# Kernel tuning notes

Measured on AMD Instinct MI355X. Metric: run time of the kernel, lower is better.

The kernel has to match this reference:

```python
import jax, jax.numpy as jnp
import numpy as np

B, S, D = 2, 2048, 1024
H = 16
HD = D // H
MLP = 4096
EPS = 1e-6


def _layernorm(x, g, b):
    mu = jnp.mean(x, axis=-1, keepdims=True)
    var = jnp.var(x, axis=-1, keepdims=True)
    return (x - mu) * jax.lax.rsqrt(var + EPS) * g + b


def setup_inputs() -> dict:
    key = jax.random.key(0)
    ks = jax.random.split(key, 16)
    sd = 1.0 / np.sqrt(D)
    sm = 1.0 / np.sqrt(MLP)
    return {
        "x": jax.random.normal(ks[0], (B, S, D), jnp.float32),
        "ln1_g": jnp.ones((D,), jnp.float32),
        "ln1_b": jnp.zeros((D,), jnp.float32),
        "wq": jax.random.normal(ks[1], (D, D), jnp.float32) * sd,
        "bq": jnp.zeros((D,), jnp.float32),
        "wk": jax.random.normal(ks[2], (D, D), jnp.float32) * sd,
        "bk": jnp.zeros((D,), jnp.float32),
        "wv": jax.random.normal(ks[3], (D, D), jnp.float32) * sd,
        "bv": jnp.zeros((D,), jnp.float32),
        "wo": jax.random.normal(ks[4], (D, D), jnp.float32) * sd,
        "bo": jnp.zeros((D,), jnp.float32),
        "ln2_g": jnp.ones((D,), jnp.float32),
        "ln2_b": jnp.zeros((D,), jnp.float32),
        "w1": jax.random.normal(ks[5], (D, MLP), jnp.float32) * sd,
        "b1": jnp.zeros((MLP,), jnp.float32),
        "w2": jax.random.normal(ks[6], (MLP, D), jnp.float32) * sm,
        "b2": jnp.zeros((D,), jnp.float32),
    }


def reference(x, ln1_g, ln1_b, wq, bq, wk, bk, wv, bv, wo, bo,
              ln2_g, ln2_b, w1, b1, w2, b2):
    # --- attention sub-block (pre-LN) ---
    h = _layernorm(x, ln1_g, ln1_b)
    q = (h @ wq + bq).reshape(B, S, H, HD).transpose(0, 2, 1, 3)  # [B,H,S,HD]
    k = (h @ wk + bk).reshape(B, S, H, HD).transpose(0, 2, 1, 3)
    v = (h @ wv + bv).reshape(B, S, H, HD).transpose(0, 2, 1, 3)
    scale = HD ** -0.5
    attn = jax.nn.softmax(jnp.einsum('bhqd,bhkd->bhqk', q, k) * scale, axis=-1)
    out = jnp.einsum('bhqk,bhkd->bhqd', attn, v)
    out = out.transpose(0, 2, 1, 3).reshape(B, S, D)
    x = x + (out @ wo + bo)
    # --- MLP sub-block (pre-LN) ---
    h = _layernorm(x, ln2_g, ln2_b)
    h = jax.nn.gelu(h @ w1 + b1, approximate=False)
    x = x + (h @ w2 + b2)
    return x
```

## Files before the change

### kernel.cpp

```cpp
#include <hip/hip_runtime.h>
#include <hip/hip_bf16.h>

typedef unsigned short u16;
typedef unsigned int u32;
typedef __attribute__((ext_vector_type(8))) unsigned short us8;
typedef __attribute__((ext_vector_type(4))) unsigned short us4;
typedef __attribute__((ext_vector_type(2))) unsigned int u32x2;
typedef __attribute__((ext_vector_type(8))) short bf16x8;
typedef __attribute__((ext_vector_type(4))) float f32x4;

#define QSCALE 0.18033688011112042f

__device__ __forceinline__ u16 f2bf(float f) {
    __hip_bfloat16 h = __float2bfloat16(f);
    return __builtin_bit_cast(u16, h);
}
__device__ __forceinline__ u32 cvtpk(float lo, float hi) {
    u32 r;
    asm("v_cvt_pk_bf16_f32 %0, %1, %2" : "=v"(r) : "v"(lo), "v"(hi));
    return r;
}
__device__ __forceinline__ float ex2(float x) {
    return __builtin_amdgcn_exp2f(x);
}
__device__ __forceinline__ float gelu7(float v) {
    const float a = v * fmaf(0.10294324f, v * v, 2.3022082f);
    const float E = ex2(a);
    return v - v * __builtin_amdgcn_rcpf(1.0f + E);
}
__device__ __forceinline__ void gll16(const u16* g, u16* l) {
    __builtin_amdgcn_global_load_lds(
        (const __attribute__((address_space(1))) unsigned int*)g,
        (__attribute__((address_space(3))) unsigned int*)l, 16, 0, 0);
}
template<int N> __device__ __forceinline__ void waitv() {
    if constexpr (N == 0)       asm volatile("s_waitcnt vmcnt(0)" ::: "memory");
    else if constexpr (N == 4)  asm volatile("s_waitcnt vmcnt(4)" ::: "memory");
    else if constexpr (N == 6)  asm volatile("s_waitcnt vmcnt(6)" ::: "memory");
    else if constexpr (N == 8)  asm volatile("s_waitcnt vmcnt(8)" ::: "memory");
    else static_assert(N == 0, "unsupported vmcnt");
}

__global__ void tcvt_k(const float* __restrict__ W, u16* __restrict__ Wt, int KK, int NN)
{
    __shared__ float tile[32][33];
    const int n0 = blockIdx.x * 32, k0 = blockIdx.y * 32;
    const int tx = threadIdx.x, ty = threadIdx.y;
    #pragma unroll
    for (int j = ty; j < 32; j += 8)
        tile[j][tx] = W[(size_t)(k0 + j) * NN + n0 + tx];
    __syncthreads();
    #pragma unroll
    for (int j = ty; j < 32; j += 8)
        Wt[(size_t)(n0 + j) * KK + k0 + tx] = f2bf(tile[tx][j]);
}

__global__ void tcvt4_k(const float* __restrict__ a, const float* __restrict__ b,
                        const float* __restrict__ c, const float* __restrict__ d,
                        u16* __restrict__ out)
{
    __shared__ float tile[32][33];
    const int z = blockIdx.z;
    const float* W = (z == 0) ? a : (z == 1) ? b : (z == 2) ? c : d;
    u16* Wt = out + (size_t)z * 1024 * 1024;
    const int n0 = blockIdx.x * 32, k0 = blockIdx.y * 32;
    const int tx = threadIdx.x, ty = threadIdx.y;
    #pragma unroll
    for (int j = ty; j < 32; j += 8)
        tile[j][tx] = W[(size_t)(k0 + j) * 1024 + n0 + tx];
    __syncthreads();
    #pragma unroll
    for (int j = ty; j < 32; j += 8)
        Wt[(size_t)(n0 + j) * 1024 + k0 + tx] = f2bf(tile[tx][j]);
}

__global__ __launch_bounds__(256) void vtr_k(const u16* __restrict__ Vb, u16* __restrict__ Vt)
{
    __shared__ u16 t[64][72];
    const int bh = blockIdx.y, s0 = blockIdx.x * 64;
    const int tid = threadIdx.x;
    const size_t ibase = (size_t)bh * 2048 * 64 + (size_t)s0 * 64;
    #pragma unroll
    for (int c = tid; c < 512; c += 256) {
        const us8 v = *(const us8*)(Vb + ibase + (size_t)(c >> 3) * 64 + (c & 7) * 8);
        *(us8*)(&t[c >> 3][(c & 7) * 8]) = v;
    }
    __syncthreads();
    const size_t obase = (size_t)bh * 64 * 2048 + s0;
    #pragma unroll
    for (int c = tid; c < 512; c += 256) {
        const int hd = c >> 3, sl0 = (c & 7) * 8;
        us8 v;
        #pragma unroll
        for (int j = 0; j < 8; j++) v[j] = t[sl0 + j][hd];
        *(us8*)(Vt + obase + (size_t)hd * 2048 + sl0) = v;
    }
}

__global__ __launch_bounds__(256) void ln_k(const float* __restrict__ x,
                                            const float* __restrict__ g,
                                            const float* __restrict__ b,
                                            u16* __restrict__ h)
{
    const int l = threadIdx.x & 63, w = threadIdx.x >> 6;
    const int row = blockIdx.x * 4 + w;
    const float* xr = x + (size_t)row * 1024;
    float4 v[4];
    float sum = 0.0f, sq = 0.0f;
    #pragma unroll
    for (int i = 0; i < 4; i++) {
        v[i] = *(const float4*)(xr + i * 256 + l * 4);
        sum += (v[i].x + v[i].y) + (v[i].z + v[i].w);
        sq  += (v[i].x * v[i].x + v[i].y * v[i].y)
             + (v[i].z * v[i].z + v[i].w * v[i].w);
    }
    #pragma unroll
    for (int off = 32; off >= 1; off >>= 1) {
        sum += __shfl_xor(sum, off);
        sq  += __shfl_xor(sq, off);
    }
    const float mean = sum * (1.0f / 1024.0f);
    const float var  = sq * (1.0f / 1024.0f) - mean * mean;
    const float inv  = rsqrtf(var + 1e-6f);
    u16* hr = h + (size_t)row * 1024;
    #pragma unroll
    for (int i = 0; i < 4; i++) {
        const int c = i * 256 + l * 4;
        us4 o;
        o[0] = f2bf((v[i].x - mean) * inv * g[c + 0] + b[c + 0]);
        o[1] = f2bf((v[i].y - mean) * inv * g[c + 1] + b[c + 1]);
        o[2] = f2bf((v[i].z - mean) * inv * g[c + 2] + b[c + 2]);
        o[3] = f2bf((v[i].w - mean) * inv * g[c + 3] + b[c + 3]);
        *(us4*)(hr + c) = o;
    }
}

template<int EPI, int TM, int BK>
__device__ __forceinline__ void gemm_body(const u16* __restrict__ A,
                                          const u16* __restrict__ Bt,
                                          const float* __restrict__ bias,
                                          void* __restrict__ outp,
                                          const float* __restrict__ addsrc,
                                          int K, float scale, int m0, int n0)
{
    constexpr int MI  = TM / 32;
    constexpr int ASZ = TM * BK;
    constexpr int BSZ = 128 * BK;
    constexpr int RPI = 512 / BK;
    constexpr int NIA = (TM / 4) / RPI;
    constexpr int NIB = 32 / RPI;
    constexpr int NI  = NIA + NIB;
    __shared__ u16 As[2 * ASZ];
    __shared__ u16 Bs[2 * BSZ];
    const int tid = threadIdx.x;
    const int l = tid & 63, w = tid >> 6;
    const int wr = w >> 1, wc = w & 1;
    const int lr = l & 15, lg = l >> 4;

    int srow, sblk;
    if constexpr (BK == 32) { srow = l >> 2; sblk = (l & 3) ^ ((l >> 3) & 3); }
    else                    { srow = l >> 3; sblk = (l & 7) ^ (l >> 3); }
    const u16* gA = A  + (size_t)(m0 + w * (TM / 4) + srow) * K + sblk * 8;
    const u16* gB = Bt + (size_t)(n0 + w * 32 + srow) * K + sblk * 8;
    const size_t rowKi = (size_t)RPI * K;
    u16* const lA0 = As + w * (TM / 4) * BK;
    u16* const lB0 = Bs + w * 32 * BK;

    f32x4 acc[MI][4];
    #pragma unroll
    for (int i = 0; i < MI; i++)
        #pragma unroll
        for (int j = 0; j < 4; j++) acc[i][j] = (f32x4)(0.0f);

    auto stage = [&](int buf, int kb) {
        u16* la = lA0 + buf * ASZ;
        u16* lb = lB0 + buf * BSZ;
        #pragma unroll
        for (int i = 0; i < NIA; i++) gll16(gA + kb + i * rowKi, la + i * 512);
        #pragma unroll
        for (int i = 0; i < NIB; i++) gll16(gB + kb + i * rowKi, lb + i * 512);
    };

    const int nK = K / BK;
    stage(0, 0);
    int cur = 0;
    for (int kt = 0; kt < nK; ++kt) {
        __builtin_amdgcn_sched_barrier(0);
        __builtin_amdgcn_s_barrier();
        __builtin_amdgcn_sched_barrier(0);
        if (kt + 1 < nK) {
            stage(cur ^ 1, (kt + 1) * BK);
            waitv<NI>();
        } else {
            waitv<0>();
        }
        __builtin_amdgcn_s_barrier();
        __builtin_amdgcn_sched_barrier(0);

        const u16* as = As + cur * ASZ;
        const u16* bs = Bs + cur * BSZ;
        #pragma unroll
        for (int ks = 0; ks < BK / 32; ks++) {
            int off;
            if constexpr (BK == 32) off = (lg ^ ((lr >> 1) & 3)) * 8;
            else                    off = ((ks * 4 + lg) ^ (lr & 7)) * 8;
            bf16x8 af[MI], bf[4];
            #pragma unroll
            for (int mi = 0; mi < MI; mi++)
                af[mi] = *(const bf16x8*)(as + (wr * (MI * 16) + mi * 16 + lr) * BK + off);
            #pragma unroll
            for (int ni = 0; ni < 4; ni++)
                bf[ni] = *(const bf16x8*)(bs + (wc * 64 + ni * 16 + lr) * BK + off);
            #pragma unroll
            for (int mi = 0; mi < MI; mi++)
                #pragma unroll
                for (int ni = 0; ni < 4; ni++)
                    acc[mi][ni] = __builtin_amdgcn_mfma_f32_16x16x32_bf16(
                        af[mi], bf[ni], acc[mi][ni], 0, 0, 0);
        }
        cur ^= 1;
    }

    const int r0 = lg * 4;
    #pragma unroll
    for (int mi = 0; mi < MI; mi++) {
        #pragma unroll
        for (int ni = 0; ni < 4; ni++) {
            const int col = n0 + wc * 64 + ni * 16 + lr;
            const float bv = bias[col];
            #pragma unroll
            for (int r = 0; r < 4; r++) {
                const int row = m0 + wr * (MI * 16) + mi * 16 + r0 + r;
                const float v = acc[mi][ni][r] + bv;
                if constexpr (EPI == 0) {
                    const int bb = row >> 11, s = row & 2047;
                    const int hh = col >> 6, hd = col & 63;
                    ((u16*)outp)[(((size_t)(bb * 16 + hh) * 2048) + s) * 64 + hd] = f2bf(v * scale);
                } else if constexpr (EPI == 1 || EPI == 3) {
                    const size_t idx = (size_t)row * 1024 + col;
                    ((float*)outp)[idx] = addsrc[idx] + v;
                } else {
                    ((u16*)outp)[(size_t)row * 4096 + col] = f2bf(gelu7(v));
                }
            }
        }
    }
}

template<int EPI, int TM, int BK, int NX>
__global__ __launch_bounds__(256) void gemm_k(const u16* __restrict__ A,
                                              const u16* __restrict__ Bt,
                                              const float* __restrict__ bias,
                                              void* __restrict__ outp,
                                              const float* __restrict__ addsrc,
                                              int K)
{
    const int nwg = gridDim.x;
    const int s = (blockIdx.x & 7) * (nwg >> 3) + (blockIdx.x >> 3);
    gemm_body<EPI, TM, BK>(A, Bt, bias, outp, addsrc, K, 1.0f,
                           (s / NX) * TM, (s % NX) * 128);
}

__global__ __launch_bounds__(256) void gemm_mlp2_k(const u16* __restrict__ A,
                                                   const u16* __restrict__ Bt,
                                                   const float* __restrict__ bias,
                                                   void* __restrict__ outp,
                                                   const float* __restrict__ addsrc,
                                                   int K)
{
    const int n = blockIdx.x & 7;
    const int m = blockIdx.x >> 3;
    gemm_body<3, 64, 64>(A, Bt, bias, outp, addsrc, K, 1.0f, m * 64, n * 128);
}

__global__ __launch_bounds__(256) void gemm_mlp1_k(const u16* __restrict__ A,
                                                   const u16* __restrict__ Bt,
                                                   const float* __restrict__ bias,
                                                   void* __restrict__ outp,
                                                   int K)
{
    const int x = blockIdx.x & 7;
    const int idx = blockIdx.x >> 3;
    const int m = (x >> 1) * 16 + (idx & 15);
    const int n = (x & 1) * 16 + (idx >> 6) * 4 + ((idx >> 4) & 3);
    gemm_body<2, 64, 64>(A, Bt, bias, outp, nullptr, K, 1.0f, m * 64, n * 128);
}

__global__ __launch_bounds__(256) void gemm_qkv_k(const u16* __restrict__ A,
                                                  const u16* __restrict__ WtBase,
                                                  const float* __restrict__ bq,
                                                  const float* __restrict__ bk,
                                                  const float* __restrict__ bv,
                                                  u16* __restrict__ outBase)
{
    const int x = blockIdx.x & 7;
    const int i = blockIdx.x >> 3;
    const int m = x * 4 + (i & 3);
    const int rest = i >> 2;
    const int z = rest >> 3, n = rest & 7;
    const u16* Bt = WtBase + (size_t)z * 1024 * 1024;
    const float* bias = (z == 0) ? bq : (z == 1) ? bk : bv;
    u16* outp = outBase + (size_t)z * 4096 * 1024;
    const float scale = (z == 0) ? QSCALE : 1.0f;
    gemm_body<0, 128, 32>(A, Bt, bias, outp, nullptr, 1024, scale,
                          m * 128, n * 128);
}

__global__ __launch_bounds__(256) void attn_mfma_k(
    const u16* __restrict__ Qb, const u16* __restrict__ Kb,
    const u16* __restrict__ Vt, u16* __restrict__ Oo)
{
    __shared__ u16 Kl[2][128 * 64];
    __shared__ u16 Vl[2][64 * 128];
    __shared__ u16 Pl[4][32 * 64];

    const int tid = threadIdx.x;
    const int l = tid & 63, w = tid >> 6;
    const int lr = l & 15, lg = l >> 4;
    const int bid = blockIdx.x;
    const int bh = (bid & 7) * 4 + ((bid >> 3) >> 4);
    const int qblk = (bid >> 3) & 15;
    const size_t base = (size_t)bh * 2048 * 64;
    const size_t vbase = (size_t)bh * 64 * 2048;
    const int q0 = qblk * 128 + w * 32;

    bf16x8 qf[2][2];
    #pragma unroll
    for (int g = 0; g < 2; g++)
        #pragma unroll
        for (int ks = 0; ks < 2; ks++)
            qf[g][ks] = *(const bf16x8*)(Qb + base + (size_t)(q0 + g * 16 + lr) * 64
                                         + ks * 32 + lg * 8);

    bf16x8 onef;
    #pragma unroll
    for (int j = 0; j < 8; j++) onef[j] = (short)0x3F80;

    f32x4 o_[2][4];
    f32x4 ol[2];
    #pragma unroll
    for (int g = 0; g < 2; g++) {
        #pragma unroll
        for (int r = 0; r < 4; r++) ol[g][r] = 0.0f;
        #pragma unroll
        for (int ni = 0; ni < 4; ni++) o_[g][ni] = (f32x4)(0.0f);
    }

    u16* const plw = &Pl[w][0];
    u16* pw_[2][4];
    const u16* pr_[2][2];
    #pragma unroll
    for (int g = 0; g < 2; g++) {
        #pragma unroll
        for (int ni = 0; ni < 4; ni++)
            pw_[g][ni] = plw + (g * 16 + lr) * 64
                       + (((ni * 2 + (lg >> 1)) ^ (lr & 7)) * 8 + (lg & 1) * 4);
        pr_[g][0] = plw + (g * 16 + lr) * 64 + ((lg ^ (lr & 7)) * 8);
        pr_[g][1] = plw + (g * 16 + lr) * 64 + (((4 + lg) ^ (lr & 7)) * 8);
    }

    const u16* gK = Kb + base + (size_t)(w * 32 + (l >> 3)) * 64
                  + (((l & 7) ^ (l >> 3)) * 8);
    u16* const kd = &Kl[0][0] + w * 32 * 64;

    const u16* gVsrc[4];
    #pragma unroll
    for (int i = 0; i < 4; i++) {
        const int vrow = w * 16 + i * 4 + (l >> 4);
        gVsrc[i] = Vt + vbase + (size_t)vrow * 2048
                 + (((l & 15) ^ (i * 4 + (l >> 4))) * 8);
    }
    u16* const vd = &Vl[0][0] + w * 16 * 128;

    auto stageT = [&](int buf, int kv) {
        u16* kdb = kd + buf * 8192;
        u16* vdb = vd + buf * 8192;
        #pragma unroll
        for (int i = 0; i < 4; i++)
            gll16(gK + (size_t)kv * 64 + i * 512, kdb + i * 512);
        #pragma unroll
        for (int i = 0; i < 4; i++)
            gll16(gVsrc[i] + kv, vdb + i * 512);
    };

    stageT(0, 0);
    int cur = 0;
    for (int t = 0; t < 16; ++t) {
        __builtin_amdgcn_sched_barrier(0);
        __builtin_amdgcn_s_barrier();
        __builtin_amdgcn_sched_barrier(0);
        if (t < 15) {
            stageT(cur ^ 1, (t + 1) * 128);
            waitv<8>();
        } else {
            waitv<0>();
        }
        __builtin_amdgcn_s_barrier();
        __builtin_amdgcn_sched_barrier(0);

        #pragma unroll
        for (int s = 0; s < 2; s++) {
            f32x4 s_[2][4];
            #pragma unroll
            for (int g = 0; g < 2; g++)
                #pragma unroll
                for (int ni = 0; ni < 4; ni++) s_[g][ni] = (f32x4)(0.0f);
            __builtin_amdgcn_s_setprio(1);
            #pragma unroll
            for (int ks = 0; ks < 2; ks++)
                #pragma unroll
                for (int ni = 0; ni < 4; ni++) {
                    const int row = ni * 16 + lr;
                    const bf16x8 kf = *(const bf16x8*)(
                        &Kl[cur][(s * 64 + row) * 64 + (((ks * 4 + lg) ^ (row & 7)) * 8)]);
                    s_[0][ni] = __builtin_amdgcn_mfma_f32_16x16x32_bf16(kf, qf[0][ks], s_[0][ni], 0, 0, 0);
                    s_[1][ni] = __builtin_amdgcn_mfma_f32_16x16x32_bf16(kf, qf[1][ks], s_[1][ni], 0, 0, 0);
                }
            __builtin_amdgcn_s_setprio(0);

            #pragma unroll
            for (int g = 0; g < 2; g++)
                #pragma unroll
                for (int ni = 0; ni < 4; ni++) {
                    u32x2 pv;
                    pv[0] = cvtpk(ex2(s_[g][ni][0]), ex2(s_[g][ni][1]));
                    pv[1] = cvtpk(ex2(s_[g][ni][2]), ex2(s_[g][ni][3]));
                    *(u32x2*)pw_[g][ni] = pv;
                }

            __builtin_amdgcn_s_setprio(1);
            #pragma unroll
            for (int ks = 0; ks < 2; ks++) {
                const bf16x8 pf0 = *(const bf16x8*)pr_[0][ks];
                const bf16x8 pf1 = *(const bf16x8*)pr_[1][ks];
                ol[0] = __builtin_amdgcn_mfma_f32_16x16x32_bf16(pf0, onef, ol[0], 0, 0, 0);
                ol[1] = __builtin_amdgcn_mfma_f32_16x16x32_bf16(pf1, onef, ol[1], 0, 0, 0);
                #pragma unroll
                for (int ni = 0; ni < 4; ni++) {
                    const int row = ni * 16 + lr;
                    const int chunk = s * 8 + ks * 4 + lg;
                    const bf16x8 vf = *(const bf16x8*)(
                        &Vl[cur][row * 128 + ((chunk ^ (row & 15)) * 8)]);
                    o_[0][ni] = __builtin_amdgcn_mfma_f32_16x16x32_bf16(pf0, vf, o_[0][ni], 0, 0, 0);
                    o_[1][ni] = __builtin_amdgcn_mfma_f32_16x16x32_bf16(pf1, vf, o_[1][ni], 0, 0, 0);
                }
            }
            __builtin_amdgcn_s_setprio(0);
        }
        cur ^= 1;
    }

    const int bb = bh >> 4, hh = bh & 15;
    #pragma unroll
    for (int g = 0; g < 2; g++)
        #pragma unroll
        for (int r = 0; r < 4; r++) {
            const float inv = 1.0f / ol[g][r];
            const int qrow = q0 + g * 16 + lg * 4 + r;
            u16* dst = Oo + ((size_t)(bb * 2048 + qrow)) * 1024 + hh * 64;
            #pragma unroll
            for (int ni = 0; ni < 4; ni++)
                dst[ni * 16 + lr] = f2bf(o_[g][ni][r] * inv);
        }
}

extern "C" void kernel_launch(void* const* d_in, const int* in_sizes, int n_in,
                              void* d_out, int out_size, void* d_ws, size_t ws_size,
                              hipStream_t stream)
{
    const float* x     = (const float*)d_in[0];
    const float* ln1_g = (const float*)d_in[1];
    const float* ln1_b = (const float*)d_in[2];
    const float* wq    = (const float*)d_in[3];
    const float* bq    = (const float*)d_in[4];
    const float* wk    = (const float*)d_in[5];
    const float* bk    = (const float*)d_in[6];
    const float* wv    = (const float*)d_in[7];
    const float* bv    = (const float*)d_in[8];
    const float* wo    = (const float*)d_in[9];
    const float* bo    = (const float*)d_in[10];
    const float* ln2_g = (const float*)d_in[11];
    const float* ln2_b = (const float*)d_in[12];
    const float* w1    = (const float*)d_in[13];
    const float* b1    = (const float*)d_in[14];
    const float* w2    = (const float*)d_in[15];
    const float* b2    = (const float*)d_in[16];

    char* ws = (char*)d_ws;
    size_t off = 0;
    auto alloc = [&](size_t bytes) {
        char* p = ws + off;
        off += (bytes + 255) & ~(size_t)255;
        return p;
    };
    u16* wtq = (u16*)alloc((size_t)1024 * 1024 * 2);
    u16* wtk = (u16*)alloc((size_t)1024 * 1024 * 2);
    u16* wtv = (u16*)alloc((size_t)1024 * 1024 * 2);
    u16* wto = (u16*)alloc((size_t)1024 * 1024 * 2);
    u16* wt1 = (u16*)alloc((size_t)4096 * 1024 * 2);
    u16* wt2 = (u16*)alloc((size_t)1024 * 4096 * 2);
    u16* h1  = (u16*)alloc((size_t)4096 * 1024 * 2);
    u16* qb  = (u16*)alloc((size_t)4096 * 1024 * 2);
    u16* kb  = (u16*)alloc((size_t)4096 * 1024 * 2);
    u16* vb  = (u16*)alloc((size_t)4096 * 1024 * 2);
    u16* ao  = (u16*)alloc((size_t)4096 * 1024 * 2);
    float* x2 = (float*)alloc((size_t)4096 * 1024 * 4);
    u16* h2  = (u16*)alloc((size_t)4096 * 1024 * 2);
    u16* mid = (u16*)alloc((size_t)4096 * 4096 * 2);
    u16* vt  = mid;
    (void)ws_size;
    (void)wtk; (void)wtv;

    const dim3 tb(32, 8);
    tcvt4_k<<<dim3(32, 32, 4), tb, 0, stream>>>(wq, wk, wv, wo, wtq);
    tcvt_k<<<dim3(128, 32), tb, 0, stream>>>(w1, wt1, 1024, 4096);
    tcvt_k<<<dim3(32, 128), tb, 0, stream>>>(w2, wt2, 4096, 1024);

    ln_k<<<1024, 256, 0, stream>>>(x, ln1_g, ln1_b, h1);

    gemm_qkv_k<<<768, 256, 0, stream>>>(h1, wtq, bq, bk, bv, qb);

    vtr_k<<<dim3(32, 32), 256, 0, stream>>>(vb, vt);
    attn_mfma_k<<<512, 256, 0, stream>>>(qb, kb, vt, ao);

    gemm_k<1, 64, 64, 8><<<512, 256, 0, stream>>>(ao, wto, bo, x2, x, 1024);

    ln_k<<<1024, 256, 0, stream>>>(x2, ln2_g, ln2_b, h2);

    gemm_mlp1_k<<<2048, 256, 0, stream>>>(h2, wt1, b1, mid, 1024);
    gemm_mlp2_k<<<512, 256, 0, stream>>>(mid, wt2, b2, (float*)d_out, x2, 4096);
}
```

Measured before the change: 240.5 us.

## Split-K the MLP down-projection with larger tiles and a separate reduction kernel

The second MLP GEMM now splits K=4096 into two halves. Each half uses a 128x128 tile with BK=32 instead of 64x128 with BK=64, so the launch still has 512 workgroups. Each split writes fp32 partial sums into the no-longer-needed q/k/v buffers, and a new elementwise kernel adds the two partials, the bias and the residual. The goal is better operand reuse per block and more parallel work in the K loop. The cost is extra global traffic to write and re-read the partial buffers, plus one more kernel launch.

```diff
diff --git a/kernel.cpp b/kernel.cpp
--- a/kernel.cpp
+++ b/kernel.cpp
@@ -141,7 +141,8 @@
                                           const float* __restrict__ bias,
                                           void* __restrict__ outp,
                                           const float* __restrict__ addsrc,
-                                          int K, float scale, int m0, int n0)
+                                          int K, int Kld, float scale,
+                                          int m0, int n0)
 {
     constexpr int MI  = TM / 32;
     constexpr int ASZ = TM * BK;
@@ -160,9 +161,9 @@
     int srow, sblk;
     if constexpr (BK == 32) { srow = l >> 2; sblk = (l & 3) ^ ((l >> 3) & 3); }
     else                    { srow = l >> 3; sblk = (l & 7) ^ (l >> 3); }
-    const u16* gA = A  + (size_t)(m0 + w * (TM / 4) + srow) * K + sblk * 8;
-    const u16* gB = Bt + (size_t)(n0 + w * 32 + srow) * K + sblk * 8;
-    const size_t rowKi = (size_t)RPI * K;
+    const u16* gA = A  + (size_t)(m0 + w * (TM / 4) + srow) * Kld + sblk * 8;
+    const u16* gB = Bt + (size_t)(n0 + w * 32 + srow) * Kld + sblk * 8;
+    const size_t rowKi = (size_t)RPI * Kld;
     u16* const lA0 = As + w * (TM / 4) * BK;
     u16* const lB0 = Bs + w * 32 * BK;
 
@@ -227,7 +228,8 @@
         #pragma unroll
         for (int ni = 0; ni < 4; ni++) {
             const int col = n0 + wc * 64 + ni * 16 + lr;
-            const float bv = bias[col];
+            float bv;
+            if constexpr (EPI == 4) bv = 0.0f; else bv = bias[col];
             #pragma unroll
             for (int r = 0; r < 4; r++) {
                 const int row = m0 + wr * (MI * 16) + mi * 16 + r0 + r;
@@ -239,8 +241,10 @@
                 } else if constexpr (EPI == 1 || EPI == 3) {
                     const size_t idx = (size_t)row * 1024 + col;
                     ((float*)outp)[idx] = addsrc[idx] + v;
+                } else if constexpr (EPI == 2) {
+                    ((u16*)outp)[(size_t)row * 4096 + col] = f2bf(gelu7(v));
                 } else {
-                    ((u16*)outp)[(size_t)row * 4096 + col] = f2bf(gelu7(v));
+                    ((float*)outp)[(size_t)row * 1024 + col] = v;
                 }
             }
         }
@@ -257,20 +261,39 @@
 {
     const int nwg = gridDim.x;
     const int s = (blockIdx.x & 7) * (nwg >> 3) + (blockIdx.x >> 3);
-    gemm_body<EPI, TM, BK>(A, Bt, bias, outp, addsrc, K, 1.0f,
+    gemm_body<EPI, TM, BK>(A, Bt, bias, outp, addsrc, K, K, 1.0f,
                            (s / NX) * TM, (s % NX) * 128);
 }
 
 __global__ __launch_bounds__(256) void gemm_mlp2_k(const u16* __restrict__ A,
                                                    const u16* __restrict__ Bt,
-                                                   const float* __restrict__ bias,
-                                                   void* __restrict__ outp,
-                                                   const float* __restrict__ addsrc,
-                                                   int K)
-{
-    const int n = blockIdx.x & 7;
-    const int m = blockIdx.x >> 3;
-    gemm_body<3, 64, 64>(A, Bt, bias, outp, addsrc, K, 1.0f, m * 64, n * 128);
+                                                   float* __restrict__ P)
+{
+    const int s = (blockIdx.x & 7) * 64 + (blockIdx.x >> 3);
+    const int kz = s >> 8, r = s & 255;
+    gemm_body<4, 128, 32>(A + kz * 2048, Bt + kz * 2048, nullptr,
+                          P + (size_t)kz * 4096 * 1024, nullptr,
+                          2048, 4096, 1.0f, (r >> 3) * 128, (r & 7) * 128);
+}
+
+__global__ __launch_bounds__(256) void mlp2_red_k(const float* __restrict__ P0,
+                                                  const float* __restrict__ P1,
+                                                  const float* __restrict__ x2,
+                                                  const float* __restrict__ b2,
+                                                  float* __restrict__ out)
+{
+    const size_t i = ((size_t)blockIdx.x * 256 + threadIdx.x) * 4;
+    const float4 a = *(const float4*)(P0 + i);
+    const float4 b = *(const float4*)(P1 + i);
+    const float4 c = *(const float4*)(x2 + i);
+    const int col = (int)(i & 1023);
+    const float4 bb = *(const float4*)(b2 + col);
+    float4 r;
+    r.x = c.x + bb.x + a.x + b.x;
+    r.y = c.y + bb.y + a.y + b.y;
+    r.z = c.z + bb.z + a.z + b.z;
+    r.w = c.w + bb.w + a.w + b.w;
+    *(float4*)(out + i) = r;
 }
 
 __global__ __launch_bounds__(256) void gemm_mlp1_k(const u16* __restrict__ A,
@@ -283,7 +306,7 @@
     const int idx = blockIdx.x >> 3;
     const int m = (x >> 1) * 16 + (idx & 15);
     const int n = (x & 1) * 16 + (idx >> 6) * 4 + ((idx >> 4) & 3);
-    gemm_body<2, 64, 64>(A, Bt, bias, outp, nullptr, K, 1.0f, m * 64, n * 128);
+    gemm_body<2, 64, 64>(A, Bt, bias, outp, nullptr, K, K, 1.0f, m * 64, n * 128);
 }
 
 __global__ __launch_bounds__(256) void gemm_qkv_k(const u16* __restrict__ A,
@@ -302,7 +325,7 @@
     const float* bias = (z == 0) ? bq : (z == 1) ? bk : bv;
     u16* outp = outBase + (size_t)z * 4096 * 1024;
     const float scale = (z == 0) ? QSCALE : 1.0f;
-    gemm_body<0, 128, 32>(A, Bt, bias, outp, nullptr, 1024, scale,
+    gemm_body<0, 128, 32>(A, Bt, bias, outp, nullptr, 1024, 1024, scale,
                           m * 128, n * 128);
 }
 
@@ -508,6 +531,8 @@
     u16* h2  = (u16*)alloc((size_t)4096 * 1024 * 2);
     u16* mid = (u16*)alloc((size_t)4096 * 4096 * 2);
     u16* vt  = mid;
+    float* p0 = (float*)qb;
+    float* p1 = (float*)vb;
     (void)ws_size;
     (void)wtk; (void)wtv;
 
@@ -528,5 +553,7 @@
     ln_k<<<1024, 256, 0, stream>>>(x2, ln2_g, ln2_b, h2);
 
     gemm_mlp1_k<<<2048, 256, 0, stream>>>(h2, wt1, b1, mid, 1024);
-    gemm_mlp2_k<<<512, 256, 0, stream>>>(mid, wt2, b2, (float*)d_out, x2, 4096);
-}
+
+    gemm_mlp2_k<<<512, 256, 0, stream>>>(mid, wt2, p0);
+    mlp2_red_k<<<4096, 256, 0, stream>>>(p0, p1, x2, b2, (float*)d_out);
+}
```

New measurement: 240.0 us. Within noise of the previous version (-0.2%).
